# Performance work log

Hardware: AMD Instinct MI355X
Metric: run time of the kernel (lower is better)

## Reference

```python
import jax, jax.numpy as jnp
import numpy as np

V, E, D, H = 50000, 800000, 128, 128  # nodes, edges, node_feat_size, graph_feat_size
NEG_SLOPE = 0.01  # nn.LeakyReLU default


def setup_inputs() -> dict:
    key = jax.random.key(0)
    ks = jax.random.split(key, 11)
    s = 0.05
    return {
        "node_feats": jax.random.normal(ks[0], (V, D), jnp.float32),
        "W_edge": jax.random.normal(ks[1], (1, 2 * D), jnp.float32) * s,
        "b_edge": jnp.zeros((1,), jnp.float32),
        "W_proj": jax.random.normal(ks[2], (H, D), jnp.float32) * s,
        "b_proj": jnp.zeros((H,), jnp.float32),
        "W_ih": jax.random.normal(ks[3], (3 * D, H), jnp.float32) * s,
        "W_hh": jax.random.normal(ks[4], (3 * D, D), jnp.float32) * s,
        "b_ih": jnp.zeros((3 * D,), jnp.float32),
        "b_hh": jnp.zeros((3 * D,), jnp.float32),
        "src": jax.random.randint(ks[5], (E,), 0, V),
        "dst": jax.random.randint(ks[6], (E,), 0, V),
    }


def _leaky_relu(x):
    return jnp.where(x >= 0, x, NEG_SLOPE * x)


def _edge_softmax(logits, dst, num_nodes):
    # segment softmax over edges grouped by destination node; logits: [E, 1]
    m = jax.ops.segment_max(logits, dst, num_segments=num_nodes)
    m = jnp.where(jnp.isfinite(m), m, 0.0)  # guard empty segments
    e = jnp.exp(logits - m[dst])
    s = jax.ops.segment_sum(e, dst, num_segments=num_nodes)
    return e / s[dst]


def reference(node_feats, W_edge, b_edge, W_proj, b_proj, W_ih, W_hh, b_ih, b_hh, src, dst):
    # GNNLayer.apply_edges: he = cat([dst_feat, src_feat])  [E, 2D]
    he = jnp.concatenate([node_feats[dst], node_feats[src]], axis=1)
    # project_edge: Dropout (eval: identity) -> Linear(2D, 1) -> LeakyReLU
    logits = _leaky_relu(he @ W_edge.T + b_edge)  # [E, 1]
    # AttentiveGRU2: edge_softmax per dst
    a = _edge_softmax(logits, dst, V)  # [E, 1]
    # project_node: Dropout (eval) -> Linear(D, H)
    hv = node_feats @ W_proj.T + b_proj  # [V, H]
    # src_mul_edge + sum aggregation to dst
    m = hv[src] * a  # [E, H]
    c = jax.ops.segment_sum(m, dst, num_segments=V)  # [V, H]
    context = jax.nn.elu(c)
    # PyTorch GRUCell(context, node_feats)
    gi = context @ W_ih.T + b_ih      # [V, 3D]
    gh = node_feats @ W_hh.T + b_hh   # [V, 3D]
    i_r, i_z, i_n = jnp.split(gi, 3, axis=1)
    h_r, h_z, h_n = jnp.split(gh, 3, axis=1)
    r = jax.nn.sigmoid(i_r + h_r)
    z = jax.nn.sigmoid(i_z + h_z)
    n = jnp.tanh(i_n + r * h_n)
    h_new = (1.0 - z) * n + z * node_feats
    return jax.nn.relu(h_new)
```

## Files before the change

kernel.cpp:

```cpp
#include <hip/hip_runtime.h>
#include <hip/hip_bf16.h>


#define V_NODES 50000
#define E_EDGES 800000
#define D_FEAT  128
#define GCHUNK  5
#define WS_BLOCKS 1250

#define NCHUNK  49
#define CHUNK_E 16384
#define RANGES  4
#define NODE_R  12500
#define HISTG   (NCHUNK * RANGES)
#define SCAN_BLOCKS 196

typedef short bf16x8 __attribute__((ext_vector_type(8)));
typedef float f32x4  __attribute__((ext_vector_type(4)));
typedef unsigned short u16x4 __attribute__((ext_vector_type(4)));

#define OFF_WEDGE 0
#define OFF_WPROJ 256
#define OFF_WIH   16640
#define OFF_WHH   65792
#define OFF_BEDGE 114944
#define OFF_BPROJ 114945
#define OFF_BIH   115073
#define OFF_BHH   115457
#define SMALL_TOTAL 115841
#define CONV_X_BLOCKS   6250
#define CONV_S_BLOCKS   453
#define HIST_BLOCKS     3125

__device__ int   g_is_bf16;
__device__ float g_pd[V_NODES];
__device__ float g_ps[V_NODES];
__device__ __attribute__((aligned(16))) unsigned int g_mat[NCHUNK * V_NODES];
__device__ int   g_row_off[V_NODES + 1];
__device__ int   g_blocksum[SCAN_BLOCKS];
__device__ int   g_blockoff[SCAN_BLOCKS];
__device__ unsigned short g_rank16[E_EDGES];
__device__ __attribute__((aligned(16))) int2 g_s_pair[E_EDGES];
__device__ __attribute__((aligned(16))) unsigned short g_xbf[V_NODES * D_FEAT];
__device__ __attribute__((aligned(16))) unsigned short g_wsmall[SMALL_TOTAL + 15];
__device__ __attribute__((aligned(16))) unsigned short g_hv[V_NODES * D_FEAT];
__device__ __attribute__((aligned(16))) unsigned short g_ctx[V_NODES * D_FEAT];

static __device__ __forceinline__ float b2f(unsigned short u) {
  union { unsigned int i; float f; } v; v.i = ((unsigned int)u) << 16; return v.f;
}
static __device__ __forceinline__ unsigned short f2b(float f) {
  unsigned int i = __float_as_uint(f);
  unsigned int r = (i + 0x7FFFu + ((i >> 16) & 1u)) >> 16;
  return (unsigned short)r;
}
static __device__ __forceinline__ bf16x8 load_frag(const unsigned short* p) {
  return *reinterpret_cast<const bf16x8*>(p);
}
static __device__ __forceinline__ float fast_rcp(float x) {
  return __builtin_amdgcn_rcpf(x);
}
static __device__ __forceinline__ float fast_sigmoid(float x) {
  return fast_rcp(1.f + __expf(-x));
}
static __device__ __forceinline__ float fast_tanh(float y) {
  return 1.f - 2.f * fast_rcp(__expf(2.f * y) + 1.f);
}

__global__ void probe_kernel(const unsigned int* __restrict__ x)
{
  __shared__ int cnt;
  if (threadIdx.x == 0) cnt = 0;
  __syncthreads();
  const unsigned int w  = x[threadIdx.x];
  const unsigned int lo = w & 0xFFFFu;
  const unsigned int ex = (lo >> 7) & 0xFFu;
  if (lo != 0u && ex >= 118u && ex <= 132u) atomicAdd(&cnt, 1);
  __syncthreads();
  if (threadIdx.x == 0) g_is_bf16 = (cnt >= 200) ? 1 : 0;
}

__global__ void conv_fused_kernel(
    const void* __restrict__ x,
    const void* p0, const void* p1, const void* p2, const void* p3,
    const void* p4, const void* p5, const void* p6, const void* p7)
{
  const int b = blockIdx.x;
  if (b < CONV_X_BLOCKS) {
    const int t = b * 256 + threadIdx.x;
    if (g_is_bf16) {
      reinterpret_cast<u16x4*>(g_xbf)[t] = reinterpret_cast<const u16x4*>(x)[t];
    } else {
      const float4 v = reinterpret_cast<const float4*>(x)[t];
      u16x4 o; o.x = f2b(v.x); o.y = f2b(v.y); o.z = f2b(v.z); o.w = f2b(v.w);
      reinterpret_cast<u16x4*>(g_xbf)[t] = o;
    }
  } else {
    const int i = (b - CONV_X_BLOCKS) * 256 + threadIdx.x;
    if (i >= SMALL_TOTAL) return;
    const int offs[9] = {OFF_WEDGE, OFF_WPROJ, OFF_WIH, OFF_WHH,
                         OFF_BEDGE, OFF_BPROJ, OFF_BIH, OFF_BHH, SMALL_TOTAL};
    const void* ps[8] = {p0, p1, p2, p3, p4, p5, p6, p7};
    int r = 0;
#pragma unroll
    for (int k = 0; k < 8; k++) if (i >= offs[k]) r = k;
    const int j = i - offs[r];
    g_wsmall[i] = g_is_bf16
        ? reinterpret_cast<const unsigned short*>(ps[r])[j]
        : f2b(reinterpret_cast<const float*>(ps[r])[j]);
  }
}

__global__ __launch_bounds__(256, 2) void np_hist_kernel(const int* __restrict__ dst)
{
  __shared__ unsigned int hloc[NODE_R / 2];
  const int b = blockIdx.x;
  if (b < HISTG) {
    const int c  = b >> 2;
    const int r0 = (b & 3) * NODE_R;
    for (int i = threadIdx.x; i < NODE_R / 2; i += 256) hloc[i] = 0u;
    __syncthreads();
    const int ebase = c * CHUNK_E;
    const int ecnt  = min(CHUNK_E, E_EDGES - ebase);
    const int4* dst4 = reinterpret_cast<const int4*>(dst + ebase);
    const int n4 = ecnt >> 2;
    for (int i = threadIdx.x; i < n4; i += 256) {
      const int4 d4 = dst4[i];
      const int e0 = ebase + (i << 2);
      const unsigned int rx = (unsigned int)(d4.x - r0);
      const unsigned int ry = (unsigned int)(d4.y - r0);
      const unsigned int rz = (unsigned int)(d4.z - r0);
      const unsigned int rw = (unsigned int)(d4.w - r0);
      if (rx < (unsigned int)NODE_R) {
        const unsigned int sh = (rx & 1u) << 4;
        const unsigned int old = atomicAdd(&hloc[rx >> 1], 1u << sh);
        g_rank16[e0] = (unsigned short)((old >> sh) & 0xFFFFu);
      }
      if (ry < (unsigned int)NODE_R) {
        const unsigned int sh = (ry & 1u) << 4;
        const unsigned int old = atomicAdd(&hloc[ry >> 1], 1u << sh);
        g_rank16[e0 + 1] = (unsigned short)((old >> sh) & 0xFFFFu);
      }
      if (rz < (unsigned int)NODE_R) {
        const unsigned int sh = (rz & 1u) << 4;
        const unsigned int old = atomicAdd(&hloc[rz >> 1], 1u << sh);
        g_rank16[e0 + 2] = (unsigned short)((old >> sh) & 0xFFFFu);
      }
      if (rw < (unsigned int)NODE_R) {
        const unsigned int sh = (rw & 1u) << 4;
        const unsigned int old = atomicAdd(&hloc[rw >> 1], 1u << sh);
        g_rank16[e0 + 3] = (unsigned short)((old >> sh) & 0xFFFFu);
      }
    }
    __syncthreads();
    uint2* mout = reinterpret_cast<uint2*>(&g_mat[c * V_NODES + r0]);
    for (int i = threadIdx.x; i < NODE_R / 2; i += 256) {
      const unsigned int w = hloc[i];
      mout[i] = make_uint2(w & 0xFFFFu, w >> 16);
    }
    return;
  }
  const int g     = (b - HISTG) * 4 + (threadIdx.x >> 6);
  const int lane  = threadIdx.x & 63;
  const int cg    = g & 7;
  const int chunk = g >> 3;
  const int col   = lane & 15;
  const int quad  = lane >> 4;
  const int h     = 16 * cg + col;

  bf16x8 bw[4];
#pragma unroll
  for (int kk = 0; kk < 4; kk++)
    bw[kk] = load_frag(g_wsmall + OFF_WPROJ + h * D_FEAT + kk * 32 + quad * 8);
  bf16x8 be[4];
#pragma unroll
  for (int kk = 0; kk < 4; kk++) { be[kk] = bf16x8{0,0,0,0,0,0,0,0}; }
  if (cg == 0 && col < 2) {
#pragma unroll
    for (int kk = 0; kk < 4; kk++)
      be[kk] = load_frag(g_wsmall + OFF_WEDGE + col * D_FEAT + kk * 32 + quad * 8);
  }
  const float bp = b2f(g_wsmall[OFF_BPROJ + h]);

  const int t0 = chunk * GCHUNK;
  bf16x8 a[4];
#pragma unroll
  for (int kk = 0; kk < 4; kk++)
    a[kk] = load_frag(g_xbf + (t0 * 16 + col) * D_FEAT + kk * 32 + quad * 8);
  for (int t = t0; t < t0 + GCHUNK; t++) {
    const int tn = (t + 1 < t0 + GCHUNK) ? t + 1 : t;
    bf16x8 na[4];
#pragma unroll
    for (int kk = 0; kk < 4; kk++)
      na[kk] = load_frag(g_xbf + (tn * 16 + col) * D_FEAT + kk * 32 + quad * 8);
    f32x4 acc; acc[0]=0.f; acc[1]=0.f; acc[2]=0.f; acc[3]=0.f;
#pragma unroll
    for (int kk = 0; kk < 4; kk++)
      acc = __builtin_amdgcn_mfma_f32_16x16x32_bf16(a[kk], bw[kk], acc, 0, 0, 0);
#pragma unroll
    for (int r = 0; r < 4; r++)
      g_hv[(t * 16 + quad * 4 + r) * D_FEAT + h] = f2b(acc[r] + bp);
    if (cg == 0) {
      f32x4 acce; acce[0]=0.f; acce[1]=0.f; acce[2]=0.f; acce[3]=0.f;
#pragma unroll
      for (int kk = 0; kk < 4; kk++)
        acce = __builtin_amdgcn_mfma_f32_16x16x32_bf16(a[kk], be[kk], acce, 0, 0, 0);
      if (col == 0) {
#pragma unroll
        for (int r = 0; r < 4; r++) g_pd[t * 16 + quad * 4 + r] = acce[r];
      } else if (col == 1) {
#pragma unroll
        for (int r = 0; r < 4; r++) g_ps[t * 16 + quad * 4 + r] = acce[r];
      }
    }
#pragma unroll
    for (int kk = 0; kk < 4; kk++) a[kk] = na[kk];
  }
}

__global__ __launch_bounds__(256) void scan_a_kernel()
{
  __shared__ int lds[256];
  const int b = blockIdx.x, t = threadIdx.x;
  const int idx = b * 256 + t;
  int v = 0;
  if (idx < V_NODES) {
#pragma unroll 7
    for (int c = 0; c < NCHUNK; c++) v += (int)g_mat[c * V_NODES + idx];
  }
  lds[t] = v;
  __syncthreads();
  for (int off = 1; off < 256; off <<= 1) {
    int tmp = (t >= off) ? lds[t - off] : 0;
    __syncthreads();
    lds[t] += tmp;
    __syncthreads();
  }
  if (idx < V_NODES) g_row_off[idx] = lds[t] - v;
  if (t == 255) g_blocksum[b] = lds[255];
}

__global__ __launch_bounds__(256) void scan_b_kernel()
{
  __shared__ int lds[256];
  const int t = threadIdx.x;
  const int v = (t < SCAN_BLOCKS) ? g_blocksum[t] : 0;
  lds[t] = v;
  __syncthreads();
  for (int off = 1; off < 256; off <<= 1) {
    int tmp = (t >= off) ? lds[t - off] : 0;
    __syncthreads();
    lds[t] += tmp;
    __syncthreads();
  }
  if (t < SCAN_BLOCKS) g_blockoff[t] = lds[t] - v;
  if (t == 255) g_row_off[V_NODES] = lds[255];
}

__global__ __launch_bounds__(256) void scan_c_kernel()
{
  const int b = blockIdx.x, t = threadIdx.x;
  const int idx = b * 256 + t;
  if (idx >= V_NODES) return;
  g_row_off[idx] += g_blockoff[b];
}

__global__ __launch_bounds__(256) void scan_m2_kernel()
{
  const int idx = blockIdx.x * 256 + threadIdx.x;
  if (idx >= V_NODES) return;
  int running = g_row_off[idx];
#pragma unroll 7
  for (int c = 0; c < NCHUNK; c++) {
    const unsigned int cnt = g_mat[c * V_NODES + idx];
    g_mat[c * V_NODES + idx] = (unsigned int)running;
    running += (int)cnt;
  }
}

__global__ void edge_scatter_kernel(
    const int* __restrict__ src, const int* __restrict__ dst, int E)
{
  int e = blockIdx.x * blockDim.x + threadIdx.x;
  if (e >= E) return;
  const int d = dst[e], sn = src[e];
  float logit = g_pd[d] + g_ps[sn] + b2f(g_wsmall[OFF_BEDGE]);
  logit = (logit >= 0.f) ? logit : 0.01f * logit;
  const float w = __expf(logit);
  const int c = e >> 14;
  const int pos = (int)g_mat[c * V_NODES + d] + (int)g_rank16[e];
  g_s_pair[pos] = make_int2(sn, __float_as_int(w));
}

__global__ __launch_bounds__(256) void aggregate_kernel()
{
  const int v = blockIdx.x * 4 + (threadIdx.x >> 6);
  const int lane = threadIdx.x & 63;
  const int beg = g_row_off[v], end = g_row_off[v + 1];
  float accx = 0.f, accy = 0.f, ssum = 0.f;
  int i = beg;
  for (; i + 4 <= end; i += 4) {
    const int2 q0 = g_s_pair[i],     q1 = g_s_pair[i + 1],
               q2 = g_s_pair[i + 2], q3 = g_s_pair[i + 3];
    const float w0 = __int_as_float(q0.y), w1 = __int_as_float(q1.y),
                w2 = __int_as_float(q2.y), w3 = __int_as_float(q3.y);
    const unsigned int p0 = *reinterpret_cast<const unsigned int*>(g_hv + q0.x * D_FEAT + lane * 2);
    const unsigned int p1 = *reinterpret_cast<const unsigned int*>(g_hv + q1.x * D_FEAT + lane * 2);
    const unsigned int p2 = *reinterpret_cast<const unsigned int*>(g_hv + q2.x * D_FEAT + lane * 2);
    const unsigned int p3 = *reinterpret_cast<const unsigned int*>(g_hv + q3.x * D_FEAT + lane * 2);
    ssum += (w0 + w1) + (w2 + w3);
    accx += w0 * b2f((unsigned short)(p0 & 0xFFFFu)) + w1 * b2f((unsigned short)(p1 & 0xFFFFu))
          + w2 * b2f((unsigned short)(p2 & 0xFFFFu)) + w3 * b2f((unsigned short)(p3 & 0xFFFFu));
    accy += w0 * b2f((unsigned short)(p0 >> 16)) + w1 * b2f((unsigned short)(p1 >> 16))
          + w2 * b2f((unsigned short)(p2 >> 16)) + w3 * b2f((unsigned short)(p3 >> 16));
  }
  for (; i < end; i++) {
    const int2 q = g_s_pair[i];
    const float w = __int_as_float(q.y);
    ssum += w;
    const unsigned int pair =
        *reinterpret_cast<const unsigned int*>(g_hv + q.x * D_FEAT + lane * 2);
    accx += w * b2f((unsigned short)(pair & 0xFFFFu));
    accy += w * b2f((unsigned short)(pair >> 16));
  }
  const float inv = (end > beg) ? (1.0f / ssum) : 0.0f;
  float c0 = accx * inv, c1 = accy * inv;
  c0 = (c0 > 0.f) ? c0 : (__expf(c0) - 1.f);
  c1 = (c1 > 0.f) ? c1 : (__expf(c1) - 1.f);
  const unsigned int outp = ((unsigned int)f2b(c1) << 16) | (unsigned int)f2b(c0);
  *reinterpret_cast<unsigned int*>(g_ctx + v * D_FEAT + lane * 2) = outp;
}

__global__ __launch_bounds__(256, 2) void gru_kernel(const float* __restrict__ xf32,
                                                     float* __restrict__ out)
{
  const int g     = blockIdx.x * 4 + (threadIdx.x >> 6);
  const int lane  = threadIdx.x & 63;
  const int cg    = g & 7;
  const int chunk = g >> 3;
  const int col   = lane & 15;
  const int quad  = lane >> 4;
  const int h     = 16 * cg + col;
  const unsigned short* W_ih = g_wsmall + OFF_WIH;
  const unsigned short* W_hh = g_wsmall + OFF_WHH;
  const int isb = g_is_bf16;

  const float br  = b2f(g_wsmall[OFF_BIH + h])       + b2f(g_wsmall[OFF_BHH + h]);
  const float bz  = b2f(g_wsmall[OFF_BIH + 128 + h]) + b2f(g_wsmall[OFF_BHH + 128 + h]);
  const float bn  = b2f(g_wsmall[OFF_BIH + 256 + h]);
  const float bh_ = b2f(g_wsmall[OFF_BHH + 256 + h]);

  bf16x8 bIHr[4], bHHr[4], bIHz[4], bHHz[4], bIHn[4], bHHn[4];
#pragma unroll
  for (int kk = 0; kk < 4; kk++) {
    const int ko = kk * 32 + quad * 8;
    bIHr[kk] = load_frag(W_ih + h * D_FEAT + ko);
    bHHr[kk] = load_frag(W_hh + h * D_FEAT + ko);
    bIHz[kk] = load_frag(W_ih + (128 + h) * D_FEAT + ko);
    bHHz[kk] = load_frag(W_hh + (128 + h) * D_FEAT + ko);
    bIHn[kk] = load_frag(W_ih + (256 + h) * D_FEAT + ko);
    bHHn[kk] = load_frag(W_hh + (256 + h) * D_FEAT + ko);
  }

  const int t0 = chunk * GCHUNK;
  for (int t = t0; t < t0 + GCHUNK; t++) {
    const int arow = t * 16 + col;
    bf16x8 ax[4], ac[4];
#pragma unroll
    for (int kk = 0; kk < 4; kk++) {
      const int o = arow * D_FEAT + kk * 32 + quad * 8;
      ax[kk] = load_frag(g_xbf + o);
      ac[kk] = load_frag(g_ctx + o);
    }
    float xv[4];
    if (isb) {
#pragma unroll
      for (int r = 0; r < 4; r++)
        xv[r] = b2f(g_xbf[(t * 16 + quad * 4 + r) * D_FEAT + h]);
    } else {
#pragma unroll
      for (int r = 0; r < 4; r++)
        xv[r] = xf32[(t * 16 + quad * 4 + r) * D_FEAT + h];
    }
    f32x4 racc, zacc, niacc, nhacc;
    racc[0]=br;  racc[1]=br;  racc[2]=br;  racc[3]=br;
    zacc[0]=bz;  zacc[1]=bz;  zacc[2]=bz;  zacc[3]=bz;
    niacc[0]=bn; niacc[1]=bn; niacc[2]=bn; niacc[3]=bn;
    nhacc[0]=bh_; nhacc[1]=bh_; nhacc[2]=bh_; nhacc[3]=bh_;
#pragma unroll
    for (int kk = 0; kk < 4; kk++) {
      racc  = __builtin_amdgcn_mfma_f32_16x16x32_bf16(ac[kk], bIHr[kk], racc, 0, 0, 0);
      racc  = __builtin_amdgcn_mfma_f32_16x16x32_bf16(ax[kk], bHHr[kk], racc, 0, 0, 0);
      zacc  = __builtin_amdgcn_mfma_f32_16x16x32_bf16(ac[kk], bIHz[kk], zacc, 0, 0, 0);
      zacc  = __builtin_amdgcn_mfma_f32_16x16x32_bf16(ax[kk], bHHz[kk], zacc, 0, 0, 0);
      niacc = __builtin_amdgcn_mfma_f32_16x16x32_bf16(ac[kk], bIHn[kk], niacc, 0, 0, 0);
      nhacc = __builtin_amdgcn_mfma_f32_16x16x32_bf16(ax[kk], bHHn[kk], nhacc, 0, 0, 0);
    }
#pragma unroll
    for (int r = 0; r < 4; r++) {
      const int vrow = t * 16 + quad * 4 + r;
      const float rg = fast_sigmoid(racc[r]);
      const float zg = fast_sigmoid(zacc[r]);
      const float n  = fast_tanh(niacc[r] + rg * nhacc[r]);
      const float hn = (1.f - zg) * n + zg * xv[r];
      out[vrow * D_FEAT + h] = (hn < 0.f) ? 0.f : hn;
    }
  }
}

extern "C" void kernel_launch(void* const* d_in, const int* in_sizes, int n_in,
                              void* d_out, int out_size, void* d_ws, size_t ws_size,
                              hipStream_t stream)
{
  (void)d_ws; (void)ws_size; (void)out_size;

  int ix = -1, iWe = -1, ibe = -1, iWp = -1, ibp = -1,
      iWih = -1, iWhh = -1, ibih = -1, ibhh = -1, isrc = -1, idst = -1;
  for (int i = 0; i < n_in; i++) {
    const int s = in_sizes[i];
    if      (s == 6400000) ix = i;
    else if (s == 256)     iWe = i;
    else if (s == 1)       ibe = i;
    else if (s == 16384)   iWp = i;
    else if (s == 128)     ibp = i;
    else if (s == 49152)   { if (iWih < 0) iWih = i; else iWhh = i; }
    else if (s == 384)     { if (ibih < 0) ibih = i; else ibhh = i; }
    else if (s == 800000)  { if (isrc < 0) isrc = i; else idst = i; }
  }
  if (ix < 0 || iWe < 0 || ibe < 0 || iWp < 0 || ibp < 0 || iWih < 0 ||
      iWhh < 0 || ibih < 0 || ibhh < 0 || isrc < 0 || idst < 0) {
    ix = 0; iWe = 1; ibe = 2; iWp = 3; ibp = 4;
    iWih = 5; iWhh = 6; ibih = 7; ibhh = 8; isrc = 9; idst = 10;
  }

  const int* src = (const int*)d_in[isrc];
  const int* dst = (const int*)d_in[idst];
  float* out = (float*)d_out;

  probe_kernel<<<1, 256, 0, stream>>>((const unsigned int*)d_in[ix]);
  conv_fused_kernel<<<CONV_X_BLOCKS + CONV_S_BLOCKS, 256, 0, stream>>>(
      d_in[ix],
      d_in[iWe], d_in[iWp], d_in[iWih], d_in[iWhh],
      d_in[ibe], d_in[ibp], d_in[ibih], d_in[ibhh]);
  np_hist_kernel<<<HISTG + WS_BLOCKS, 256, 0, stream>>>(dst);
  scan_a_kernel<<<SCAN_BLOCKS, 256, 0, stream>>>();
  scan_b_kernel<<<1, 256, 0, stream>>>();
  scan_c_kernel<<<SCAN_BLOCKS, 256, 0, stream>>>();
  scan_m2_kernel<<<SCAN_BLOCKS, 256, 0, stream>>>();
  edge_scatter_kernel<<<HIST_BLOCKS, 256, 0, stream>>>(src, dst, E_EDGES);
  aggregate_kernel<<<V_NODES / 4, 256, 0, stream>>>();
  gru_kernel<<<WS_BLOCKS, 256, 0, stream>>>((const float*)d_in[ix], out);
}
```

Baseline: 238.3 us.

## Split GRU kernel reduction across wave pairs with LDS partial-sum exchange

Each GRU task is now split over two waves that each handle half of the K dimension. Partial MFMA accumulators are combined through double-buffered shared memory, and only one wave applies the gate nonlinearities and writes the output. This halves per-wave weight-fragment registers, raises the occupancy hint, and doubles the block count to add latency hiding. In exchange it adds a block-wide barrier per tile, LDS traffic, and idle epilogue waves.

```diff
diff --git a/kernel.cpp b/kernel.cpp
--- a/kernel.cpp
+++ b/kernel.cpp
@@ -7,6 +7,7 @@
 #define D_FEAT  128
 #define GCHUNK  5
 #define WS_BLOCKS 1250
+#define GRU_BLOCKS 2500
 
 #define NCHUNK  49
 #define CHUNK_E 16384
@@ -331,13 +332,17 @@
   *reinterpret_cast<unsigned int*>(g_ctx + v * D_FEAT + lane * 2) = outp;
 }
 
-__global__ __launch_bounds__(256, 2) void gru_kernel(const float* __restrict__ xf32,
+__global__ __launch_bounds__(256, 3) void gru_kernel(const float* __restrict__ xf32,
                                                      float* __restrict__ out)
 {
-  const int g     = blockIdx.x * 4 + (threadIdx.x >> 6);
+  __shared__ float part[2][2][16][64];
+  const int wid   = threadIdx.x >> 6;
   const int lane  = threadIdx.x & 63;
-  const int cg    = g & 7;
-  const int chunk = g >> 3;
+  const int ks    = wid >> 1;
+  const int cgs   = wid & 1;
+  const int task  = blockIdx.x * 2 + cgs;
+  const int cg    = task & 7;
+  const int chunk = task >> 3;
   const int col   = lane & 15;
   const int quad  = lane >> 4;
   const int h     = 16 * cg + col;
@@ -345,42 +350,47 @@
   const unsigned short* W_hh = g_wsmall + OFF_WHH;
   const int isb = g_is_bf16;
 
-  const float br  = b2f(g_wsmall[OFF_BIH + h])       + b2f(g_wsmall[OFF_BHH + h]);
-  const float bz  = b2f(g_wsmall[OFF_BIH + 128 + h]) + b2f(g_wsmall[OFF_BHH + 128 + h]);
-  const float bn  = b2f(g_wsmall[OFF_BIH + 256 + h]);
-  const float bh_ = b2f(g_wsmall[OFF_BHH + 256 + h]);
-
-  bf16x8 bIHr[4], bHHr[4], bIHz[4], bHHz[4], bIHn[4], bHHn[4];
-#pragma unroll
-  for (int kk = 0; kk < 4; kk++) {
-    const int ko = kk * 32 + quad * 8;
-    bIHr[kk] = load_frag(W_ih + h * D_FEAT + ko);
-    bHHr[kk] = load_frag(W_hh + h * D_FEAT + ko);
-    bIHz[kk] = load_frag(W_ih + (128 + h) * D_FEAT + ko);
-    bHHz[kk] = load_frag(W_hh + (128 + h) * D_FEAT + ko);
-    bIHn[kk] = load_frag(W_ih + (256 + h) * D_FEAT + ko);
-    bHHn[kk] = load_frag(W_hh + (256 + h) * D_FEAT + ko);
+  float br = 0.f, bz = 0.f, bn = 0.f, bh_ = 0.f;
+  if (ks == 0) {
+    br  = b2f(g_wsmall[OFF_BIH + h])       + b2f(g_wsmall[OFF_BHH + h]);
+    bz  = b2f(g_wsmall[OFF_BIH + 128 + h]) + b2f(g_wsmall[OFF_BHH + 128 + h]);
+    bn  = b2f(g_wsmall[OFF_BIH + 256 + h]);
+    bh_ = b2f(g_wsmall[OFF_BHH + 256 + h]);
+  }
+
+  bf16x8 bIHr[2], bHHr[2], bIHz[2], bHHz[2], bIHn[2], bHHn[2];
+#pragma unroll
+  for (int j = 0; j < 2; j++) {
+    const int ko = (2 * ks + j) * 32 + quad * 8;
+    bIHr[j] = load_frag(W_ih + h * D_FEAT + ko);
+    bHHr[j] = load_frag(W_hh + h * D_FEAT + ko);
+    bIHz[j] = load_frag(W_ih + (128 + h) * D_FEAT + ko);
+    bHHz[j] = load_frag(W_hh + (128 + h) * D_FEAT + ko);
+    bIHn[j] = load_frag(W_ih + (256 + h) * D_FEAT + ko);
+    bHHn[j] = load_frag(W_hh + (256 + h) * D_FEAT + ko);
   }
 
   const int t0 = chunk * GCHUNK;
   for (int t = t0; t < t0 + GCHUNK; t++) {
     const int arow = t * 16 + col;
-    bf16x8 ax[4], ac[4];
-#pragma unroll
-    for (int kk = 0; kk < 4; kk++) {
-      const int o = arow * D_FEAT + kk * 32 + quad * 8;
-      ax[kk] = load_frag(g_xbf + o);
-      ac[kk] = load_frag(g_ctx + o);
+    bf16x8 ax[2], ac[2];
+#pragma unroll
+    for (int j = 0; j < 2; j++) {
+      const int o = arow * D_FEAT + (2 * ks + j) * 32 + quad * 8;
+      ax[j] = load_frag(g_xbf + o);
+      ac[j] = load_frag(g_ctx + o);
     }
     float xv[4];
-    if (isb) {
-#pragma unroll
-      for (int r = 0; r < 4; r++)
-        xv[r] = b2f(g_xbf[(t * 16 + quad * 4 + r) * D_FEAT + h]);
-    } else {
-#pragma unroll
-      for (int r = 0; r < 4; r++)
-        xv[r] = xf32[(t * 16 + quad * 4 + r) * D_FEAT + h];
+    if (ks == 0) {
+      if (isb) {
+#pragma unroll
+        for (int r = 0; r < 4; r++)
+          xv[r] = b2f(g_xbf[(t * 16 + quad * 4 + r) * D_FEAT + h]);
+      } else {
+#pragma unroll
+        for (int r = 0; r < 4; r++)
+          xv[r] = xf32[(t * 16 + quad * 4 + r) * D_FEAT + h];
+      }
     }
     f32x4 racc, zacc, niacc, nhacc;
     racc[0]=br;  racc[1]=br;  racc[2]=br;  racc[3]=br;
@@ -388,22 +398,42 @@
     niacc[0]=bn; niacc[1]=bn; niacc[2]=bn; niacc[3]=bn;
     nhacc[0]=bh_; nhacc[1]=bh_; nhacc[2]=bh_; nhacc[3]=bh_;
 #pragma unroll
-    for (int kk = 0; kk < 4; kk++) {
-      racc  = __builtin_amdgcn_mfma_f32_16x16x32_bf16(ac[kk], bIHr[kk], racc, 0, 0, 0);
-      racc  = __builtin_amdgcn_mfma_f32_16x16x32_bf16(ax[kk], bHHr[kk], racc, 0, 0, 0);
-      zacc  = __builtin_amdgcn_mfma_f32_16x16x32_bf16(ac[kk], bIHz[kk], zacc, 0, 0, 0);
-      zacc  = __builtin_amdgcn_mfma_f32_16x16x32_bf16(ax[kk], bHHz[kk], zacc, 0, 0, 0);
-      niacc = __builtin_amdgcn_mfma_f32_16x16x32_bf16(ac[kk], bIHn[kk], niacc, 0, 0, 0);
-      nhacc = __builtin_amdgcn_mfma_f32_16x16x32_bf16(ax[kk], bHHn[kk], nhacc, 0, 0, 0);
-    }
-#pragma unroll
-    for (int r = 0; r < 4; r++) {
-      const int vrow = t * 16 + quad * 4 + r;
-      const float rg = fast_sigmoid(racc[r]);
-      const float zg = fast_sigmoid(zacc[r]);
-      const float n  = fast_tanh(niacc[r] + rg * nhacc[r]);
-      const float hn = (1.f - zg) * n + zg * xv[r];
-      out[vrow * D_FEAT + h] = (hn < 0.f) ? 0.f : hn;
+    for (int j = 0; j < 2; j++) {
+      racc  = __builtin_amdgcn_mfma_f32_16x16x32_bf16(ac[j], bIHr[j], racc, 0, 0, 0);
+      racc  = __builtin_amdgcn_mfma_f32_16x16x32_bf16(ax[j], bHHr[j], racc, 0, 0, 0);
+      zacc  = __builtin_amdgcn_mfma_f32_16x16x32_bf16(ac[j], bIHz[j], zacc, 0, 0, 0);
+      zacc  = __builtin_amdgcn_mfma_f32_16x16x32_bf16(ax[j], bHHz[j], zacc, 0, 0, 0);
+      niacc = __builtin_amdgcn_mfma_f32_16x16x32_bf16(ac[j], bIHn[j], niacc, 0, 0, 0);
+      nhacc = __builtin_amdgcn_mfma_f32_16x16x32_bf16(ax[j], bHHn[j], nhacc, 0, 0, 0);
+    }
+    const int buf = t & 1;
+    if (ks == 1) {
+#pragma unroll
+      for (int r = 0; r < 4; r++) {
+        part[buf][cgs][r][lane]      = racc[r];
+        part[buf][cgs][4 + r][lane]  = zacc[r];
+        part[buf][cgs][8 + r][lane]  = niacc[r];
+        part[buf][cgs][12 + r][lane] = nhacc[r];
+      }
+    }
+    __syncthreads();
+    if (ks == 0) {
+#pragma unroll
+      for (int r = 0; r < 4; r++) {
+        racc[r]  += part[buf][cgs][r][lane];
+        zacc[r]  += part[buf][cgs][4 + r][lane];
+        niacc[r] += part[buf][cgs][8 + r][lane];
+        nhacc[r] += part[buf][cgs][12 + r][lane];
+      }
+#pragma unroll
+      for (int r = 0; r < 4; r++) {
+        const int vrow = t * 16 + quad * 4 + r;
+        const float rg = fast_sigmoid(racc[r]);
+        const float zg = fast_sigmoid(zacc[r]);
+        const float n  = fast_tanh(niacc[r] + rg * nhacc[r]);
+        const float hn = (1.f - zg) * n + zg * xv[r];
+        out[vrow * D_FEAT + h] = (hn < 0.f) ? 0.f : hn;
+      }
     }
   }
 }
@@ -449,5 +479,5 @@
   scan_m2_kernel<<<SCAN_BLOCKS, 256, 0, stream>>>();
   edge_scatter_kernel<<<HIST_BLOCKS, 256, 0, stream>>>(src, dst, E_EDGES);
   aggregate_kernel<<<V_NODES / 4, 256, 0, stream>>>();
-  gru_kernel<<<WS_BLOCKS, 256, 0, stream>>>((const float*)d_in[ix], out);
-}
+  gru_kernel<<<GRU_BLOCKS, 256, 0, stream>>>((const float*)d_in[ix], out);
+}
```

Measured after the change: 240.2 us. Within noise of the previous version (+0.8%).

## Fuse scan stages into one kernel and remap GRU blocks by chunk halves

Applied to the files above, without the earlier changes.

Merges the single-block block-sum scan, the offset-add pass and the per-chunk prefix pass into one kernel. Each of the 196 blocks redundantly rescans the 196 block sums in LDS, which removes two launches and a global round trip for the block offsets. Separately, the GRU grid is remapped so that each block covers half of the column groups of a chunk, with an XCD-aware interleave of block ids. The grid is padded to 1264 blocks and the surplus blocks exit early, presumably to improve L2 locality of node rows across the chiplets.

```diff
diff --git a/kernel.cpp b/kernel.cpp
--- a/kernel.cpp
+++ b/kernel.cpp
@@ -7,6 +7,7 @@
 #define D_FEAT  128
 #define GCHUNK  5
 #define WS_BLOCKS 1250
+#define GRU_BLOCKS 1264
 
 #define NCHUNK  49
 #define CHUNK_E 16384
@@ -38,7 +39,6 @@
 __device__ __attribute__((aligned(16))) unsigned int g_mat[NCHUNK * V_NODES];
 __device__ int   g_row_off[V_NODES + 1];
 __device__ int   g_blocksum[SCAN_BLOCKS];
-__device__ int   g_blockoff[SCAN_BLOCKS];
 __device__ unsigned short g_rank16[E_EDGES];
 __device__ __attribute__((aligned(16))) int2 g_s_pair[E_EDGES];
 __device__ __attribute__((aligned(16))) unsigned short g_xbf[V_NODES * D_FEAT];
@@ -240,10 +240,10 @@
   if (t == 255) g_blocksum[b] = lds[255];
 }
 
-__global__ __launch_bounds__(256) void scan_b_kernel()
+__global__ __launch_bounds__(256) void scan_bcm_kernel()
 {
   __shared__ int lds[256];
-  const int t = threadIdx.x;
+  const int b = blockIdx.x, t = threadIdx.x;
   const int v = (t < SCAN_BLOCKS) ? g_blocksum[t] : 0;
   lds[t] = v;
   __syncthreads();
@@ -253,29 +253,20 @@
     lds[t] += tmp;
     __syncthreads();
   }
-  if (t < SCAN_BLOCKS) g_blockoff[t] = lds[t] - v;
-  if (t == 255) g_row_off[V_NODES] = lds[255];
-}
-
-__global__ __launch_bounds__(256) void scan_c_kernel()
-{
-  const int b = blockIdx.x, t = threadIdx.x;
+  const int total = lds[255];
+  const int boff  = (b == 0) ? 0 : lds[b - 1];
   const int idx = b * 256 + t;
-  if (idx >= V_NODES) return;
-  g_row_off[idx] += g_blockoff[b];
-}
-
-__global__ __launch_bounds__(256) void scan_m2_kernel()
-{
-  const int idx = blockIdx.x * 256 + threadIdx.x;
-  if (idx >= V_NODES) return;
-  int running = g_row_off[idx];
+  if (idx < V_NODES) {
+    int running = g_row_off[idx] + boff;
+    g_row_off[idx] = running;
 #pragma unroll 7
-  for (int c = 0; c < NCHUNK; c++) {
-    const unsigned int cnt = g_mat[c * V_NODES + idx];
-    g_mat[c * V_NODES + idx] = (unsigned int)running;
-    running += (int)cnt;
-  }
+    for (int c = 0; c < NCHUNK; c++) {
+      const unsigned int cnt = g_mat[c * V_NODES + idx];
+      g_mat[c * V_NODES + idx] = (unsigned int)running;
+      running += (int)cnt;
+    }
+  }
+  if (b == 0 && t == 0) g_row_off[V_NODES] = total;
 }
 
 __global__ void edge_scatter_kernel(
@@ -334,10 +325,15 @@
 __global__ __launch_bounds__(256, 2) void gru_kernel(const float* __restrict__ xf32,
                                                      float* __restrict__ out)
 {
-  const int g     = blockIdx.x * 4 + (threadIdx.x >> 6);
+  const int d = blockIdx.x;
+  const int x = d & 7;
+  const int s = d >> 3;
+  const int chunk = x + 8 * (s >> 1);
+  if (chunk >= 625) return;
+  const int half  = s & 1;
+  const int wid   = threadIdx.x >> 6;
   const int lane  = threadIdx.x & 63;
-  const int cg    = g & 7;
-  const int chunk = g >> 3;
+  const int cg    = half * 4 + wid;
   const int col   = lane & 15;
   const int quad  = lane >> 4;
   const int h     = 16 * cg + col;
@@ -444,10 +440,8 @@
       d_in[ibe], d_in[ibp], d_in[ibih], d_in[ibhh]);
   np_hist_kernel<<<HISTG + WS_BLOCKS, 256, 0, stream>>>(dst);
   scan_a_kernel<<<SCAN_BLOCKS, 256, 0, stream>>>();
-  scan_b_kernel<<<1, 256, 0, stream>>>();
-  scan_c_kernel<<<SCAN_BLOCKS, 256, 0, stream>>>();
-  scan_m2_kernel<<<SCAN_BLOCKS, 256, 0, stream>>>();
+  scan_bcm_kernel<<<SCAN_BLOCKS, 256, 0, stream>>>();
   edge_scatter_kernel<<<HIST_BLOCKS, 256, 0, stream>>>(src, dst, E_EDGES);
   aggregate_kernel<<<V_NODES / 4, 256, 0, stream>>>();
-  gru_kernel<<<WS_BLOCKS, 256, 0, stream>>>((const float*)d_in[ix], out);
-}
+  gru_kernel<<<GRU_BLOCKS, 256, 0, stream>>>((const float*)d_in[ix], out);
+}
```

Result: no change. 233.9 us (-1.8%).
